# Optimization experiments

Measured on AMD Instinct MI355X. Metric: run time of the kernel, lower is better.

## Reference

```python
import jax, jax.numpy as jnp
import numpy as np

K = 30  # top-k spatial positions kept per channel


def setup_inputs() -> dict:
    key = jax.random.key(0)
    k1, k2, k3 = jax.random.split(key, 3)
    b, c, h, w = 32, 384, 56, 56
    x = jax.random.normal(k1, (b, c, h, w), dtype=jnp.float32)
    # depthwise conv: torch weight shape (C, 1, 3, 3), bias (C,)
    fan_in = 1 * 3 * 3
    bound = 1.0 / np.sqrt(fan_in)
    weight = jax.random.uniform(k2, (c, 1, 3, 3), dtype=jnp.float32, minval=-bound, maxval=bound)
    bias = jax.random.uniform(k3, (c,), dtype=jnp.float32, minval=-bound, maxval=bound)
    return {"x": x, "weight": weight, "bias": bias}


def reference(x, weight, bias):
    b, c, h, w = x.shape
    # depthwise 3x3 conv, padding=1 (SAME), groups=c
    scores = jax.lax.conv_general_dilated(
        x, weight,
        window_strides=(1, 1),
        padding="SAME",
        feature_group_count=c,
        dimension_numbers=("NCHW", "OIHW", "NCHW"),
    ) + bias[None, :, None, None]
    scores_flat = scores.reshape(b, c, h * w)
    _, topk_idx = jax.lax.top_k(scores_flat, K)  # (b, c, K)
    bi = jnp.arange(b)[:, None, None]
    ci = jnp.arange(c)[None, :, None]
    mask = jnp.zeros((b, c, h * w), dtype=x.dtype).at[bi, ci, topk_idx].set(1.0)
    return x * mask.reshape(b, c, h, w)
```

## Files before the change

kernel.cpp:

```cpp
#include <hip/hip_runtime.h>

#define NT 256
#define W 56
#define HW 3136
#define KSEL 30
#define CAP 160

typedef float v2f __attribute__((ext_vector_type(2)));

__device__ __forceinline__ v2f vfma(v2f a, v2f b, v2f c) {
#if __has_builtin(__builtin_elementwise_fma)
    return __builtin_elementwise_fma(a, b, c);
#else
    v2f r; r.x = fmaf(a.x, b.x, c.x); r.y = fmaf(a.y, b.y, c.y); return r;
#endif
}

__global__ __launch_bounds__(NT, 8) void topk_spatial_kernel(
    const float* __restrict__ x,
    const float* __restrict__ wgt,
    const float* __restrict__ bias,
    float* __restrict__ out,
    int C)
{
    __shared__ unsigned int smax[NT];
    __shared__ int          c_idx[CAP];
    __shared__ double       c_sd[CAP];
    __shared__ unsigned int keepw[HW / 32];
    __shared__ unsigned int s_T16;
    __shared__ int s_cnt;

    const int tid = threadIdx.x;
    const int bc  = blockIdx.x;
    const int ci  = bc % C;

    const float* xp = x   + (size_t)bc * HW;
    float*       op = out + (size_t)bc * HW;

    const float* wpt = wgt + (size_t)ci * 9;
    const float wk[3][3] = { { wpt[0], wpt[1], wpt[2] },
                             { wpt[3], wpt[4], wpt[5] },
                             { wpt[6], wpt[7], wpt[8] } };
    const float bv = bias[ci];

    if (tid < HW / 32) keepw[tid] = 0u;
    if (tid == 255) s_cnt = 0;

    const int m_ = tid & 15;
    const int g_ = tid >> 4;
    const bool active = (m_ < 14) && (g_ < 14);
    const int mq = (m_ < 14) ? m_ : 13;
    const int gq = (g_ < 14) ? g_ : 13;

    unsigned int k32[16];
    unsigned int mx = 0u;
    {
        v2f accL[4], accH[4];
        #pragma unroll
        for (int k = 0; k < 4; ++k) { accL[k] = v2f{bv, bv}; accH[k] = v2f{bv, bv}; }

        const int cb = 4 * mq;
        #pragma unroll
        for (int dr = 0; dr < 6; ++dr) {
            const int rr = 4 * gq - 1 + dr;
            const int ra = (rr < 0) ? 0 : ((rr > 55) ? 55 : rr);
            const bool rok = (rr >= 0) && (rr < 56);
            float4 vm = *reinterpret_cast<const float4*>(xp + ra * W + cb);
            vm.x = rok ? vm.x : 0.0f;
            vm.y = rok ? vm.y : 0.0f;
            vm.z = rok ? vm.z : 0.0f;
            vm.w = rok ? vm.w : 0.0f;
            const float lraw = __shfl_up(vm.w, 1);
            const float rraw = __shfl_down(vm.x, 1);
            const float vl = (m_ == 0)  ? 0.0f : lraw;
            const float vr = (m_ == 13) ? 0.0f : rraw;

            const v2f p0 = { vl,   vm.x };
            const v2f p1 = { vm.x, vm.y };
            const v2f p2 = { vm.y, vm.z };
            const v2f p3 = { vm.z, vm.w };
            const v2f p4 = { vm.w, vr   };
            #pragma unroll
            for (int k = 0; k < 4; ++k) {
                const int kr = dr - k;
                if (kr >= 0 && kr < 3) {
                    const v2f wA = { wk[kr][0], wk[kr][0] };
                    const v2f wB = { wk[kr][1], wk[kr][1] };
                    const v2f wC = { wk[kr][2], wk[kr][2] };
                    accL[k] = vfma(wA, p0, accL[k]);
                    accL[k] = vfma(wB, p1, accL[k]);
                    accL[k] = vfma(wC, p2, accL[k]);
                    accH[k] = vfma(wA, p2, accH[k]);
                    accH[k] = vfma(wB, p3, accH[k]);
                    accH[k] = vfma(wC, p4, accH[k]);
                }
            }
        }

        if (active) {
            #pragma unroll
            for (int k = 0; k < 4; ++k) {
                const float sv[4] = { accL[k].x, accL[k].y, accH[k].x, accH[k].y };
                #pragma unroll
                for (int j = 0; j < 4; ++j) {
                    const unsigned int bb = __float_as_uint(sv[j]);
                    const unsigned int key = ((int)bb < 0) ? ~bb : (bb | 0x80000000u);
                    k32[k * 4 + j] = key;
                    mx = (key > mx) ? key : mx;
                }
            }
        } else {
            #pragma unroll
            for (int kk = 0; kk < 16; ++kk) k32[kk] = 0u;
        }
    }

    smax[tid] = mx;
    __syncthreads();

    if (tid < 64) {
        const unsigned int m0 = smax[tid]       >> 16;
        const unsigned int m1 = smax[tid + 64]  >> 16;
        const unsigned int m2 = smax[tid + 128] >> 16;
        const unsigned int m3 = smax[tid + 192] >> 16;
        unsigned int lo = 0u, hi = 65536u;
        while (hi - lo > 1u) {
            const unsigned int mid = (lo + hi) >> 1;
            const int c = (m0 >= mid) + (m1 >= mid) + (m2 >= mid) + (m3 >= mid);
            const unsigned long long b0 = __ballot(c & 1);
            const unsigned long long b1 = __ballot(c & 2);
            const unsigned long long b2 = __ballot(c & 4);
            const int cnt = __popcll(b0) + 2 * __popcll(b1) + 4 * __popcll(b2);
            if (cnt >= KSEL) { lo = mid; if (cnt <= 48) break; }
            else hi = mid;
        }
        if (tid == 0) s_T16 = lo;
    }
    __syncthreads();

    const unsigned int binkey = s_T16 << 16;
    const float Tf = (binkey & 0x80000000u)
                         ? __uint_as_float(binkey ^ 0x80000000u)
                         : __uint_as_float(~binkey);
    const float Tm = Tf - 1e-4f;
    const unsigned int tb    = __float_as_uint(Tm);
    const unsigned int TmKey = ((int)tb < 0) ? ~tb : (tb | 0x80000000u);

    if (active) {
        #pragma unroll
        for (int kk = 0; kk < 16; ++kk) {
            if (k32[kk] >= TmKey) {
                const int slot = atomicAdd(&s_cnt, 1);
                if (slot < CAP)
                    c_idx[slot] = (4 * g_ + (kk >> 2)) * W + 4 * m_ + (kk & 3);
            }
        }
    }
    __syncthreads();

    const int E = (s_cnt < CAP) ? s_cnt : CAP;
    if (tid < E) {
        const int i  = c_idx[tid];
        const int y  = i / W;
        const int xc = i - y * W;
        double s = (double)bv;
        #pragma unroll
        for (int dy = -1; dy <= 1; ++dy) {
            #pragma unroll
            for (int dx = -1; dx <= 1; ++dx) {
                const int yy = y + dy, xx = xc + dx;
                const int ya = (yy < 0) ? 0 : ((yy > 55) ? 55 : yy);
                const int xa = (xx < 0) ? 0 : ((xx > 55) ? 55 : xx);
                const float xv = xp[ya * W + xa];
                const bool ok = ((unsigned)yy < 56u) && ((unsigned)xx < 56u);
                s = fma((double)wk[dy + 1][dx + 1], ok ? (double)xv : 0.0, s);
            }
        }
        c_sd[tid] = s;
    }
    __syncthreads();

    if (tid < E) {
        const double se = c_sd[tid];
        const int    ei = c_idx[tid];
        int rank = 0;
        for (int j = 0; j < E; ++j) {
            const double sj = c_sd[j];
            const int    ji = c_idx[j];
            rank += (sj > se) || (sj == se && ji < ei);
        }
        if (rank < KSEL) atomicOr(&keepw[ei >> 5], 1u << (ei & 31));
    }
    __syncthreads();

    if (active) {
        #pragma unroll
        for (int k = 0; k < 4; ++k) {
            const int ib = (4 * g_ + k) * W + 4 * m_;
            float4 v = *reinterpret_cast<const float4*>(xp + ib);
            const unsigned int bits = keepw[ib >> 5] >> (ib & 31);
            v.x = (bits & 1u) ? v.x : 0.0f;
            v.y = (bits & 2u) ? v.y : 0.0f;
            v.z = (bits & 4u) ? v.z : 0.0f;
            v.w = (bits & 8u) ? v.w : 0.0f;
            *reinterpret_cast<float4*>(&op[ib]) = v;
        }
    }
}

extern "C" void kernel_launch(void* const* d_in, const int* in_sizes, int n_in,
                              void* d_out, int out_size, void* d_ws, size_t ws_size,
                              hipStream_t stream) {
    const float* x  = (const float*)d_in[0];
    const float* w  = (const float*)d_in[1];
    const float* b  = (const float*)d_in[2];
    float* out      = (float*)d_out;

    const int C  = in_sizes[2];
    const int BC = in_sizes[0] / HW;

    topk_spatial_kernel<<<BC, NT, 0, stream>>>(x, w, b, out, C);
}
```

Before: 99.64 us.

## Keep tile rows in registers and share halo rows via LDS

Each thread now loads its four rows of the 4x4 tile once into registers and reuses them both for the depthwise conv and for the final masked store. Halo rows above and below come from neighbours through two shared-memory arrays instead of extra global loads. This removes the redundant global reads (six row loads plus four reloads per thread) at the cost of one extra barrier, more LDS and more live registers, which may reduce occupancy under the 8-wave launch bound.

```diff
diff --git a/kernel.cpp b/kernel.cpp
--- a/kernel.cpp
+++ b/kernel.cpp
@@ -23,6 +23,8 @@
     float* __restrict__ out,
     int C)
 {
+    __shared__ float4       hsA[14][14];
+    __shared__ float4       hsB[14][14];
     __shared__ unsigned int smax[NT];
     __shared__ int          c_idx[CAP];
     __shared__ double       c_sd[CAP];
@@ -43,15 +45,27 @@
                              { wpt[6], wpt[7], wpt[8] } };
     const float bv = bias[ci];
 
-    if (tid < HW / 32) keepw[tid] = 0u;
-    if (tid == 255) s_cnt = 0;
-
     const int m_ = tid & 15;
     const int g_ = tid >> 4;
     const bool active = (m_ < 14) && (g_ < 14);
     const int mq = (m_ < 14) ? m_ : 13;
     const int gq = (g_ < 14) ? g_ : 13;
 
+    if (tid < HW / 32) keepw[tid] = 0u;
+    if (tid == 255) s_cnt = 0;
+
+    float4 xm[4];
+    #pragma unroll
+    for (int k = 0; k < 4; ++k) xm[k] = float4{0.f, 0.f, 0.f, 0.f};
+    if (active) {
+        #pragma unroll
+        for (int k = 0; k < 4; ++k)
+            xm[k] = *reinterpret_cast<const float4*>(xp + (4 * g_ + k) * W + 4 * m_);
+        hsA[g_][m_] = xm[3];
+        hsB[g_][m_] = xm[0];
+    }
+    __syncthreads();
+
     unsigned int k32[16];
     unsigned int mx = 0u;
     {
@@ -59,17 +73,18 @@
         #pragma unroll
         for (int k = 0; k < 4; ++k) { accL[k] = v2f{bv, bv}; accH[k] = v2f{bv, bv}; }
 
-        const int cb = 4 * mq;
+        const float4 haloT = hsA[(gq > 0) ? gq - 1 : 0][mq];
+        const float4 haloB = hsB[(gq < 13) ? gq + 1 : 13][mq];
+
         #pragma unroll
         for (int dr = 0; dr < 6; ++dr) {
-            const int rr = 4 * gq - 1 + dr;
-            const int ra = (rr < 0) ? 0 : ((rr > 55) ? 55 : rr);
-            const bool rok = (rr >= 0) && (rr < 56);
-            float4 vm = *reinterpret_cast<const float4*>(xp + ra * W + cb);
-            vm.x = rok ? vm.x : 0.0f;
-            vm.y = rok ? vm.y : 0.0f;
-            vm.z = rok ? vm.z : 0.0f;
-            vm.w = rok ? vm.w : 0.0f;
+            float4 vm;
+            if (dr == 0)      vm = haloT;
+            else if (dr == 5) vm = haloB;
+            else              vm = xm[dr - 1];
+            if (dr == 0 && g_ == 0)  vm = float4{0.f, 0.f, 0.f, 0.f};
+            if (dr == 5 && g_ == 13) vm = float4{0.f, 0.f, 0.f, 0.f};
+
             const float lraw = __shfl_up(vm.w, 1);
             const float rraw = __shfl_down(vm.x, 1);
             const float vl = (m_ == 0)  ? 0.0f : lraw;
@@ -197,8 +212,8 @@
         #pragma unroll
         for (int k = 0; k < 4; ++k) {
             const int ib = (4 * g_ + k) * W + 4 * m_;
-            float4 v = *reinterpret_cast<const float4*>(xp + ib);
             const unsigned int bits = keepw[ib >> 5] >> (ib & 31);
+            float4 v = xm[k];
             v.x = (bits & 1u) ? v.x : 0.0f;
             v.y = (bits & 2u) ? v.y : 0.0f;
             v.z = (bits & 4u) ? v.z : 0.0f;
```

Result: faster. 84.66 us (-15.0%).
